# Kernel tuning notes

Measured on AMD Instinct MI355X. Metric: run time of the kernel, lower is better.

Reference implementation:

```python
import jax, jax.numpy as jnp
import numpy as np

SELF_OBS_DIM = 18
NBR_OBS_DIM = 6
NUM_NBR = 8
HID = 128

def _mlp2(x, W1, b1, W2, b2):
    return jnp.tanh(jnp.tanh(x @ W1 + b1) @ W2 + b2)

def setup_inputs() -> dict:
    key = jax.random.key(0)
    ks = jax.random.split(key, 20)
    B = 65536
    def w(k, i, o):
        return (jax.random.normal(k, (i, o), jnp.float32) / np.sqrt(i)).astype(jnp.float32)
    inp = {
        "self_obs": jax.random.normal(ks[0], (B, SELF_OBS_DIM), jnp.float32),
        "obs": jax.random.normal(ks[1], (B, SELF_OBS_DIM + NUM_NBR * NBR_OBS_DIM), jnp.float32),
        # embedding_mlp
        "e_W1": w(ks[2], SELF_OBS_DIM + NBR_OBS_DIM, HID), "e_b1": jnp.zeros((HID,), jnp.float32),
        "e_W2": w(ks[3], HID, HID), "e_b2": jnp.zeros((HID,), jnp.float32),
        # neighbor_value_mlp
        "v_W1": w(ks[4], HID, HID), "v_b1": jnp.zeros((HID,), jnp.float32),
        "v_W2": w(ks[5], HID, HID), "v_b2": jnp.zeros((HID,), jnp.float32),
        # attention_mlp
        "a_W1": w(ks[6], 2 * HID, HID), "a_b1": jnp.zeros((HID,), jnp.float32),
        "a_W2": w(ks[7], HID, HID), "a_b2": jnp.zeros((HID,), jnp.float32),
        "a_W3": w(ks[8], HID, 1), "a_b3": jnp.zeros((1,), jnp.float32),
        "all_neighbor_obs_size": NUM_NBR * NBR_OBS_DIM,
        "batch_size": B,
    }
    return inp

def reference(self_obs, obs, e_W1, e_b1, e_W2, e_b2, v_W1, v_b1, v_W2, v_b2,
              a_W1, a_b1, a_W2, a_b2, a_W3, a_b3, all_neighbor_obs_size, batch_size):
    B = batch_size
    n = NUM_NBR
    # slice out neighbor obs; reshape is batch-major: row index = b*n + k
    obs_nb = obs[:, SELF_OBS_DIM:SELF_OBS_DIM + all_neighbor_obs_size].reshape(-1, NBR_OBS_DIM)
    # torch .repeat(n, 1) tiles whole batch -> neighbor-major: row index = k*B + b (kept faithful)
    self_rep = jnp.tile(self_obs, (n, 1))
    emb = _mlp2(jnp.concatenate([self_rep, obs_nb], axis=1), e_W1, e_b1, e_W2, e_b2)  # [B*n, H]
    vals = _mlp2(emb, v_W1, v_b1, v_W2, v_b2)                                          # [B*n, H]
    emb_mean = emb.reshape(B, n, HID).mean(axis=1)                                     # [B, H]
    mean_rep = jnp.tile(emb_mean, (n, 1))                                              # [B*n, H]
    h = jnp.tanh(jnp.concatenate([emb, mean_rep], axis=1) @ a_W1 + a_b1)
    h = jnp.tanh(h @ a_W2 + a_b2)
    scores = (h @ a_W3 + a_b3).reshape(B, n)
    attn = jax.nn.softmax(scores, axis=1).reshape(-1, 1)
    out = (attn * vals).reshape(B, n, HID).sum(axis=1)                                 # [B, H]
    return out
```

## Files before the change

kernel.cpp:

```cpp
#include <hip/hip_runtime.h>
#include <math.h>

#define BATCH 65536
#define HID   128
#define NTHREADS 256

using bf16x8 = __attribute__((ext_vector_type(8))) short;
using f32x4  = __attribute__((ext_vector_type(4))) float;

#define E1H 0
#define E1L 4096
#define SWB 8192
#define BIASF 204800
#define MEANH 206592
#define WS_ELEMS_FULL (MEANH + BATCH*HID)

__device__ __forceinline__ float4 ld4(const float* p) { return *reinterpret_cast<const float4*>(p); }

__device__ __forceinline__ unsigned cvtpk(float a, float b) {
    unsigned r;
    asm("v_cvt_pk_bf16_f32 %0, %1, %2" : "=v"(r) : "v"(a), "v"(b));
    return r;
}

__device__ __forceinline__ float tanh_f(float x) {
    float t = __builtin_amdgcn_exp2f(x * 2.8853900817779268f);
    float r = __builtin_amdgcn_rcpf(t + 1.f);
    return 1.f - 2.f * r;
}

__device__ __forceinline__ f32x4 mfma16(bf16x8 a, bf16x8 b, f32x4 c) {
    return __builtin_amdgcn_mfma_f32_16x16x32_bf16(a, b, c, 0, 0, 0);
}

__device__ __forceinline__ bf16x8 pk8(unsigned u0, unsigned u1, unsigned u2, unsigned u3) {
    union { unsigned u[4]; bf16x8 v; } x;
    x.u[0] = u0; x.u[1] = u1; x.u[2] = u2; x.u[3] = u3;
    return x.v;
}

__device__ __forceinline__ void split_pack(float v0, float v1, float v2, float v3,
        unsigned& uh0, unsigned& uh1, unsigned& ul0, unsigned& ul1) {
    uh0 = cvtpk(v0, v1); uh1 = cvtpk(v2, v3);
    float f0 = __uint_as_float(uh0 << 16), f1 = __uint_as_float(uh0 & 0xffff0000u);
    float f2 = __uint_as_float(uh1 << 16), f3 = __uint_as_float(uh1 & 0xffff0000u);
    ul0 = cvtpk(v0 - f0, v1 - f1); ul1 = cvtpk(v2 - f2, v3 - f3);
}

__device__ __forceinline__ void zacc(f32x4 acc[2][8]) {
    #pragma unroll
    for (int rt = 0; rt < 2; ++rt)
        #pragma unroll
        for (int t = 0; t < 8; ++t) acc[rt][t] = f32x4{0.f, 0.f, 0.f, 0.f};
}

__device__ __forceinline__ int permc(int p) {
    return 32 * ((p >> 4) & 3) + 8 * ((p >> 2) & 3) + 4 * (p >> 6) + (p & 3);
}

__device__ __forceinline__ void gload16(const void* g, void* l) {
    __builtin_amdgcn_global_load_lds(
        (const __attribute__((address_space(1))) void*)g,
        (__attribute__((address_space(3))) void*)l, 16, 0, 0);
}
__device__ __forceinline__ void stage32k(short* dst, const short* __restrict__ src, int tid) {
    const char* g = (const char*)src + tid * 16;
    char* l = (char*)dst + tid * 16;
    #pragma unroll
    for (int s = 0; s < 8; ++s) gload16(g + s * 4096, l + s * 4096);
}

template<int NMUL>
__device__ __forceinline__ void mm_half(f32x4 acc[2][8],
        const bf16x8 Bh[2][4], const bf16x8 Bl[2][4],
        const short* W, int sE, int sO)
{
    #pragma unroll
    for (int tp = 0; tp < 4; ++tp) {
        const int t0 = 2 * tp, t1 = t0 + 1;
        __builtin_amdgcn_s_setprio(1);
        #pragma unroll
        for (int ks = 0; ks < 4; ++ks) {
            const int base = ((ks & 1) ? sO : sE) + (ks >> 1) * 64 + tp * 4096;
            bf16x8 w0 = *(const bf16x8*)(W + base);
            bf16x8 w1 = *(const bf16x8*)(W + base + 2048);
            acc[0][t0] = mfma16(w0, Bh[0][ks], acc[0][t0]);
            acc[0][t1] = mfma16(w1, Bh[0][ks], acc[0][t1]);
            acc[1][t0] = mfma16(w0, Bh[1][ks], acc[1][t0]);
            acc[1][t1] = mfma16(w1, Bh[1][ks], acc[1][t1]);
            if (NMUL == 2) {
                acc[0][t0] = mfma16(w0, Bl[0][ks], acc[0][t0]);
                acc[0][t1] = mfma16(w1, Bl[0][ks], acc[0][t1]);
                acc[1][t0] = mfma16(w0, Bl[1][ks], acc[1][t0]);
                acc[1][t1] = mfma16(w1, Bl[1][ks], acc[1][t1]);
            }
        }
        __builtin_amdgcn_s_setprio(0);
    }
}

__device__ __forceinline__ void mm_l1(f32x4 acc[2][8],
        const bf16x8 X0h[2], const bf16x8 X0l[2],
        const short* __restrict__ Wh, const short* __restrict__ Wl, int wb)
{
    #pragma unroll
    for (int tp = 0; tp < 4; ++tp) {
        const short* whp = Wh + wb + tp * 1024;
        const short* wlp = Wl + wb + tp * 1024;
        bf16x8 wh0 = *(const bf16x8*)(whp);
        bf16x8 wh1 = *(const bf16x8*)(whp + 512);
        bf16x8 wl0 = *(const bf16x8*)(wlp);
        bf16x8 wl1 = *(const bf16x8*)(wlp + 512);
        __builtin_amdgcn_s_setprio(1);
        acc[0][2*tp  ] = mfma16(wh0, X0h[0], acc[0][2*tp  ]);
        acc[0][2*tp+1] = mfma16(wh1, X0h[0], acc[0][2*tp+1]);
        acc[1][2*tp  ] = mfma16(wh0, X0h[1], acc[1][2*tp  ]);
        acc[1][2*tp+1] = mfma16(wh1, X0h[1], acc[1][2*tp+1]);
        acc[0][2*tp  ] = mfma16(wh0, X0l[0], acc[0][2*tp  ]);
        acc[0][2*tp+1] = mfma16(wh1, X0l[0], acc[0][2*tp+1]);
        acc[1][2*tp  ] = mfma16(wh0, X0l[1], acc[1][2*tp  ]);
        acc[1][2*tp+1] = mfma16(wh1, X0l[1], acc[1][2*tp+1]);
        acc[0][2*tp  ] = mfma16(wl0, X0h[0], acc[0][2*tp  ]);
        acc[0][2*tp+1] = mfma16(wl1, X0h[0], acc[0][2*tp+1]);
        acc[1][2*tp  ] = mfma16(wl0, X0h[1], acc[1][2*tp  ]);
        acc[1][2*tp+1] = mfma16(wl1, X0h[1], acc[1][2*tp+1]);
        __builtin_amdgcn_s_setprio(0);
    }
}

__device__ __forceinline__ void epi_state(const f32x4 acc[2][8], const float* __restrict__ bp,
        int q4, bf16x8 Nh[2][4], bf16x8 Nl[2][4])
{
    #pragma unroll
    for (int ks = 0; ks < 4; ++ks) {
        float4 b0 = ld4(bp + 16 * ks + q4);
        float4 b1 = ld4(bp + 16 * ks + 64 + q4);
        #pragma unroll
        for (int rt = 0; rt < 2; ++rt) {
            unsigned h0, h1, h2, h3, l0, l1, l2, l3;
            split_pack(tanh_f(acc[rt][ks][0] + b0.x), tanh_f(acc[rt][ks][1] + b0.y),
                       tanh_f(acc[rt][ks][2] + b0.z), tanh_f(acc[rt][ks][3] + b0.w),
                       h0, h1, l0, l1);
            split_pack(tanh_f(acc[rt][ks+4][0] + b1.x), tanh_f(acc[rt][ks+4][1] + b1.y),
                       tanh_f(acc[rt][ks+4][2] + b1.z), tanh_f(acc[rt][ks+4][3] + b1.w),
                       h2, h3, l2, l3);
            Nh[rt][ks] = pk8(h0, h1, h2, h3);
            Nl[rt][ks] = pk8(l0, l1, l2, l3);
        }
    }
}

__device__ __forceinline__ void epi_state_hi(const f32x4 acc[2][8], const float* __restrict__ bp,
        int q4, bf16x8 Nh[2][4])
{
    #pragma unroll
    for (int ks = 0; ks < 4; ++ks) {
        float4 b0 = ld4(bp + 16 * ks + q4);
        float4 b1 = ld4(bp + 16 * ks + 64 + q4);
        #pragma unroll
        for (int rt = 0; rt < 2; ++rt) {
            unsigned h0 = cvtpk(tanh_f(acc[rt][ks][0] + b0.x), tanh_f(acc[rt][ks][1] + b0.y));
            unsigned h1 = cvtpk(tanh_f(acc[rt][ks][2] + b0.z), tanh_f(acc[rt][ks][3] + b0.w));
            unsigned h2 = cvtpk(tanh_f(acc[rt][ks+4][0] + b1.x), tanh_f(acc[rt][ks+4][1] + b1.y));
            unsigned h3 = cvtpk(tanh_f(acc[rt][ks+4][2] + b1.z), tanh_f(acc[rt][ks+4][3] + b1.w));
            Nh[rt][ks] = pk8(h0, h1, h2, h3);
        }
    }
}

__device__ __forceinline__ void build_x0(bf16x8 X0h[2], bf16x8 X0l[2],
        const float* __restrict__ self_obs, const float* __restrict__ obs,
        int r0w, int lm, int q)
{
    #pragma unroll
    for (int rt = 0; rt < 2; ++rt) {
        int row = r0w + 16 * rt + lm;
        const float* sp = self_obs + (size_t)(row & (BATCH - 1)) * 18;
        float x0 = 0.f, x1 = 0.f, x2 = 0.f, x3 = 0.f, x4 = 0.f, x5 = 0.f, x6 = 0.f, x7 = 0.f;
        if (q == 0) {
            x0 = sp[0]; x1 = sp[1]; x2 = sp[2]; x3 = sp[3];
            x4 = sp[4]; x5 = sp[5]; x6 = sp[6]; x7 = sp[7];
        } else if (q == 1) {
            x0 = sp[8]; x1 = sp[9]; x2 = sp[10]; x3 = sp[11];
            x4 = sp[12]; x5 = sp[13]; x6 = sp[14]; x7 = sp[15];
        } else if (q == 2) {
            x0 = sp[16]; x1 = sp[17];
            const float* op = obs + (size_t)(row >> 3) * 66 + 18 + (row & 7) * 6;
            x2 = op[0]; x3 = op[1]; x4 = op[2]; x5 = op[3]; x6 = op[4]; x7 = op[5];
        }
        unsigned h0, h1, h2, h3, l0, l1, l2, l3;
        split_pack(x0, x1, x2, x3, h0, h1, l0, l1);
        split_pack(x4, x5, x6, x7, h2, h3, l2, l3);
        X0h[rt] = pk8(h0, h1, h2, h3);
        X0l[rt] = pk8(l0, l1, l2, l3);
    }
}

__device__ __forceinline__ int remap(int hw) {
    return (((hw >> 3) & 7) << 9) | ((hw & 7) << 6) | (hw >> 6);
}

__global__ void prep_w(const float* __restrict__ eW1, const float* __restrict__ eW2,
                       const float* __restrict__ vW1, const float* __restrict__ vW2,
                       const float* __restrict__ aW1, const float* __restrict__ aW2,
                       const float* __restrict__ eb1, const float* __restrict__ eb2,
                       const float* __restrict__ vb1, const float* __restrict__ vb2,
                       const float* __restrict__ ab1, const float* __restrict__ ab2,
                       const float* __restrict__ aW3,
                       short* __restrict__ ws)
{
    int t = blockIdx.x * blockDim.x + threadIdx.x;
    if (t >= 103296) return;
    if (t >= 102400) {
        int i = t - 102400, arr = i >> 7, p = i & 127;
        int c = permc(p);
        float v;
        if      (arr == 0) v = eb1[c];
        else if (arr == 1) v = eb2[c];
        else if (arr == 2) v = vb1[c];
        else if (arr == 3) v = vb2[c];
        else if (arr == 4) v = ab1[c];
        else if (arr == 5) v = ab2[c];
        else               v = aW3[c];
        ((float*)(ws + BIASF))[arr * 128 + p] = v;
        return;
    }
    float v; int dh, dl;
    if (t < 4096) {
        int p = t >> 5, k = t & 31;
        v = (k < 24) ? eW1[k * HID + permc(p)] : 0.f;
        dh = E1H + t; dl = E1L + t;
    } else {
        int u = t - 4096;
        int blob = u >> 14, vv = u & 16383;
        int p = vv >> 7;
        int k = (vv & 127) ^ ((p & 7) << 3);
        int c = permc(p);
        if      (blob == 0) v = eW2[k * HID + c];
        else if (blob == 1) v = aW1[k * HID + c];
        else if (blob == 2) v = aW1[(128 + k) * HID + c];
        else if (blob == 3) v = aW2[k * HID + c];
        else if (blob == 4) v = vW1[k * HID + c];
        else                v = vW2[k * HID + c];
        dh = SWB + blob * 32768 + vv;
        dl = dh + 16384;
    }
    unsigned uu = __float_as_uint(v);
    unsigned h = (uu + 0x7fffu + ((uu >> 16) & 1u)) >> 16;
    float lf = v - __uint_as_float(h << 16);
    ws[dh] = (short)h;
    ws[dl] = (short)(__float_as_uint(lf) >> 16);
}

__global__ __launch_bounds__(NTHREADS, 2)
void qk_mean(const float* __restrict__ self_obs, const float* __restrict__ obs,
             short* ws)
{
    __shared__ __align__(16) short B0[16384], B1[16384];
    const int tid = threadIdx.x, lane = tid & 63;
    const int lm = lane & 15, q = lane >> 4;
    const int r0w = remap(blockIdx.x) * 128 + (tid >> 6) * 32;
    const float* bf = (const float*)(ws + BIASF);
    const int sE = (lm * 128 + 8 * q) ^ ((lm & 7) << 3);
    const int sO = (lm * 128 + 8 * q + 32) ^ ((lm & 7) << 3);

    stage32k(B0, ws + SWB, tid);

    f32x4 acc[2][8];
    bf16x8 X0h[2], X0l[2];
    build_x0(X0h, X0l, self_obs, obs, r0w, lm, q);
    zacc(acc);
    mm_l1(acc, X0h, X0l, ws + E1H, ws + E1L, lm * 32 + q * 8);
    bf16x8 Hh[2][4], Hl[2][4];
    epi_state(acc, bf, q * 4, Hh, Hl);
    __syncthreads();

    stage32k(B1, ws + SWB + 16384, tid);
    zacc(acc);
    mm_half<2>(acc, Hh, Hl, B0, sE, sO);
    __syncthreads();
    mm_half<1>(acc, Hh, Hh, B1, sE, sO);

    const float* b2 = bf + 128;
    short* mh = ws + MEANH;
    #pragma unroll
    for (int rt = 0; rt < 2; ++rt) {
        float m[8][4];
        #pragma unroll
        for (int ks = 0; ks < 4; ++ks) {
            float4 b0 = ld4(b2 + 16 * ks + 4 * q);
            float4 b1 = ld4(b2 + 16 * ks + 64 + 4 * q);
            m[ks][0] = tanh_f(acc[rt][ks][0] + b0.x);
            m[ks][1] = tanh_f(acc[rt][ks][1] + b0.y);
            m[ks][2] = tanh_f(acc[rt][ks][2] + b0.z);
            m[ks][3] = tanh_f(acc[rt][ks][3] + b0.w);
            m[ks+4][0] = tanh_f(acc[rt][ks+4][0] + b1.x);
            m[ks+4][1] = tanh_f(acc[rt][ks+4][1] + b1.y);
            m[ks+4][2] = tanh_f(acc[rt][ks+4][2] + b1.z);
            m[ks+4][3] = tanh_f(acc[rt][ks+4][3] + b1.w);
        }
        #pragma unroll
        for (int t = 0; t < 8; ++t)
            #pragma unroll
            for (int e = 0; e < 4; ++e) {
                float v = m[t][e];
                v += __shfl_xor(v, 1); v += __shfl_xor(v, 2); v += __shfl_xor(v, 4);
                m[t][e] = v * 0.125f;
            }
        if ((lm & 7) == 0) {
            int g = (r0w >> 3) + 2 * rt + (lm >> 3);
            #pragma unroll
            for (int ks = 0; ks < 4; ++ks) {
                unsigned h0 = cvtpk(m[ks][0], m[ks][1]);
                unsigned h1 = cvtpk(m[ks][2], m[ks][3]);
                unsigned h2 = cvtpk(m[ks+4][0], m[ks+4][1]);
                unsigned h3 = cvtpk(m[ks+4][2], m[ks+4][3]);
                *(bf16x8*)(mh + (size_t)g * 128 + 32 * ks + 8 * q) = pk8(h0, h1, h2, h3);
            }
        }
    }
}

__global__ __launch_bounds__(NTHREADS, 2)
void qk_main(const float* __restrict__ self_obs, const float* __restrict__ obs,
             short* ws, float* __restrict__ out)
{
    __shared__ __align__(16) short B0[16384], B1[16384];
    const int tid = threadIdx.x, lane = tid & 63;
    const int lm = lane & 15, q = lane >> 4;
    const int r0w = remap(blockIdx.x) * 128 + (tid >> 6) * 32;
    const float* bf = (const float*)(ws + BIASF);
    const int sE = (lm * 128 + 8 * q) ^ ((lm & 7) << 3);
    const int sO = (lm * 128 + 8 * q + 32) ^ ((lm & 7) << 3);
    const short* W = ws + SWB;

    f32x4 acc[2][8];
    float a0, a1;

    stage32k(B0, W, tid);
    {
        bf16x8 X0h[2], X0l[2];
        build_x0(X0h, X0l, self_obs, obs, r0w, lm, q);
        zacc(acc);
        mm_l1(acc, X0h, X0l, ws + E1H, ws + E1L, lm * 32 + q * 8);
    }
    bf16x8 Hh[2][4], Hl[2][4];
    epi_state(acc, bf, q * 4, Hh, Hl);
    __syncthreads();

    stage32k(B1, W + 1 * 16384, tid);
    zacc(acc);
    mm_half<2>(acc, Hh, Hl, B0, sE, sO);
    __syncthreads();
    stage32k(B0, W + 2 * 16384, tid);
    mm_half<1>(acc, Hh, Hh, B1, sE, sO);
    bf16x8 Eh[2][4], El[2][4];
    epi_state(acc, bf + 128, q * 4, Eh, El);
    __syncthreads();

    stage32k(B1, W + 3 * 16384, tid);
    zacc(acc);
    mm_half<2>(acc, Eh, El, B0, sE, sO);
    __syncthreads();
    stage32k(B0, W + 4 * 16384, tid);
    bf16x8 Mh[2][4];
    {
        const short* mh = ws + MEANH;
        const size_t mr0 = (size_t)((r0w + lm) & (BATCH - 1)) * 128;
        const size_t mr1 = (size_t)((r0w + 16 + lm) & (BATCH - 1)) * 128;
        #pragma unroll
        for (int ks = 0; ks < 4; ++ks) {
            Mh[0][ks] = *(const bf16x8*)(mh + mr0 + 32 * ks + 8 * q);
            Mh[1][ks] = *(const bf16x8*)(mh + mr1 + 32 * ks + 8 * q);
        }
    }
    mm_half<1>(acc, Eh, Eh, B1, sE, sO);
    __syncthreads();

    stage32k(B1, W + 5 * 16384, tid);
    mm_half<1>(acc, Mh, Mh, B0, sE, sO);
    __syncthreads();
    stage32k(B0, W + 6 * 16384, tid);
    mm_half<1>(acc, Mh, Mh, B1, sE, sO);
    bf16x8 Ah[2][4];
    epi_state_hi(acc, bf + 4 * 128, q * 4, Ah);
    __syncthreads();

    stage32k(B1, W + 7 * 16384, tid);
    zacc(acc);
    mm_half<1>(acc, Ah, Ah, B0, sE, sO);
    __syncthreads();
    stage32k(B0, W + 8 * 16384, tid);
    mm_half<1>(acc, Ah, Ah, B1, sE, sO);
    {
        const float* b6  = bf + 5 * 128;
        const float* w3p = bf + 6 * 128;
        float p0 = 0.f, p1 = 0.f;
        #pragma unroll
        for (int t = 0; t < 8; ++t) {
            float4 b  = ld4(b6 + 16 * t + 4 * q);
            float4 wv = ld4(w3p + 16 * t + 4 * q);
            p0 += tanh_f(acc[0][t][0] + b.x) * wv.x + tanh_f(acc[0][t][1] + b.y) * wv.y
                + tanh_f(acc[0][t][2] + b.z) * wv.z + tanh_f(acc[0][t][3] + b.w) * wv.w;
            p1 += tanh_f(acc[1][t][0] + b.x) * wv.x + tanh_f(acc[1][t][1] + b.y) * wv.y
                + tanh_f(acc[1][t][2] + b.z) * wv.z + tanh_f(acc[1][t][3] + b.w) * wv.w;
        }
        p0 += __shfl_xor(p0, 16); p0 += __shfl_xor(p0, 32);
        p1 += __shfl_xor(p1, 16); p1 += __shfl_xor(p1, 32);
        float m0 = p0, m1 = p1;
        m0 = fmaxf(m0, __shfl_xor(m0, 1)); m0 = fmaxf(m0, __shfl_xor(m0, 2)); m0 = fmaxf(m0, __shfl_xor(m0, 4));
        m1 = fmaxf(m1, __shfl_xor(m1, 1)); m1 = fmaxf(m1, __shfl_xor(m1, 2)); m1 = fmaxf(m1, __shfl_xor(m1, 4));
        float e0 = __expf(p0 - m0), e1 = __expf(p1 - m1);
        float s0 = e0, s1 = e1;
        s0 += __shfl_xor(s0, 1); s0 += __shfl_xor(s0, 2); s0 += __shfl_xor(s0, 4);
        s1 += __shfl_xor(s1, 1); s1 += __shfl_xor(s1, 2); s1 += __shfl_xor(s1, 4);
        a0 = e0 * __builtin_amdgcn_rcpf(s0);
        a1 = e1 * __builtin_amdgcn_rcpf(s1);
    }
    __syncthreads();

    stage32k(B1, W + 9 * 16384, tid);
    zacc(acc);
    mm_half<2>(acc, Eh, El, B0, sE, sO);
    __syncthreads();
    stage32k(B0, W + 10 * 16384, tid);
    mm_half<1>(acc, Eh, Eh, B1, sE, sO);
    bf16x8 Vh[2][4], Vl[2][4];
    epi_state(acc, bf + 2 * 128, q * 4, Vh, Vl);
    __syncthreads();

    stage32k(B1, W + 11 * 16384, tid);
    zacc(acc);
    mm_half<2>(acc, Vh, Vl, B0, sE, sO);
    __syncthreads();
    mm_half<1>(acc, Vh, Vh, B1, sE, sO);
    const float* b4 = bf + 3 * 128;
    #pragma unroll
    for (int rt = 0; rt < 2; ++rt) {
        const float av = rt ? a1 : a0;
        float o[8][4];
        #pragma unroll
        for (int ks = 0; ks < 4; ++ks) {
            float4 b0 = ld4(b4 + 16 * ks + 4 * q);
            float4 b1 = ld4(b4 + 16 * ks + 64 + 4 * q);
            o[ks][0] = av * tanh_f(acc[rt][ks][0] + b0.x);
            o[ks][1] = av * tanh_f(acc[rt][ks][1] + b0.y);
            o[ks][2] = av * tanh_f(acc[rt][ks][2] + b0.z);
            o[ks][3] = av * tanh_f(acc[rt][ks][3] + b0.w);
            o[ks+4][0] = av * tanh_f(acc[rt][ks+4][0] + b1.x);
            o[ks+4][1] = av * tanh_f(acc[rt][ks+4][1] + b1.y);
            o[ks+4][2] = av * tanh_f(acc[rt][ks+4][2] + b1.z);
            o[ks+4][3] = av * tanh_f(acc[rt][ks+4][3] + b1.w);
        }
        #pragma unroll
        for (int t = 0; t < 8; ++t)
            #pragma unroll
            for (int e = 0; e < 4; ++e) {
                float v = o[t][e];
                v += __shfl_xor(v, 1); v += __shfl_xor(v, 2); v += __shfl_xor(v, 4);
                o[t][e] = v;
            }
        if ((lm & 7) == 0) {
            int g = (r0w >> 3) + 2 * rt + (lm >> 3);
            #pragma unroll
            for (int ks = 0; ks < 4; ++ks) {
                *(float4*)(out + (size_t)g * 128 + 32 * ks + 8 * q) =
                    make_float4(o[ks][0], o[ks][1], o[ks][2], o[ks][3]);
                *(float4*)(out + (size_t)g * 128 + 32 * ks + 8 * q + 4) =
                    make_float4(o[ks+4][0], o[ks+4][1], o[ks+4][2], o[ks+4][3]);
            }
        }
    }
}

extern "C" void kernel_launch(void* const* d_in, const int* in_sizes, int n_in,
                              void* d_out, int out_size, void* d_ws, size_t ws_size,
                              hipStream_t stream) {
    const float* self_obs = (const float*)d_in[0];
    const float* obs      = (const float*)d_in[1];
    const float* eW1 = (const float*)d_in[2];  const float* eb1 = (const float*)d_in[3];
    const float* eW2 = (const float*)d_in[4];  const float* eb2 = (const float*)d_in[5];
    const float* vW1 = (const float*)d_in[6];  const float* vb1 = (const float*)d_in[7];
    const float* vW2 = (const float*)d_in[8];  const float* vb2 = (const float*)d_in[9];
    const float* aW1 = (const float*)d_in[10]; const float* ab1 = (const float*)d_in[11];
    const float* aW2 = (const float*)d_in[12]; const float* ab2 = (const float*)d_in[13];
    const float* aW3 = (const float*)d_in[14];
    float* out = (float*)d_out;
    short* ws = (short*)d_ws;

    prep_w<<<404, 256, 0, stream>>>(eW1, eW2, vW1, vW2, aW1, aW2,
                                    eb1, eb2, vb1, vb2, ab1, ab2, aW3, ws);

    dim3 grid(4096);
    qk_mean<<<grid, NTHREADS, 0, stream>>>(self_obs, obs, ws);
    qk_main<<<grid, NTHREADS, 0, stream>>>(self_obs, obs, ws, out);
}
```

Measured before the change: 389.9 us.

## Split weight staging into quarter tiles to halve LDS in qk_mean

The qk_mean kernel now double-buffers weights in 16 KB quarter-layer chunks instead of 32 KB halves, so LDS per block drops from 64 KB to 32 KB. A new layer4/mm_q path overlaps each quarter's global-to-LDS load with the MFMA work on the previous quarter. This allows more resident blocks and finer overlap, at the cost of more barriers and more setprio toggling per layer.

```diff
diff --git a/kernel.cpp b/kernel.cpp
--- a/kernel.cpp
+++ b/kernel.cpp
@@ -63,11 +63,65 @@
         (const __attribute__((address_space(1))) void*)g,
         (__attribute__((address_space(3))) void*)l, 16, 0, 0);
 }
+__device__ __forceinline__ void stage16k(short* dst, const short* __restrict__ src, int tid) {
+    const char* g = (const char*)src + tid * 16;
+    char* l = (char*)dst + tid * 16;
+    #pragma unroll
+    for (int s = 0; s < 4; ++s) gload16(g + s * 4096, l + s * 4096);
+}
 __device__ __forceinline__ void stage32k(short* dst, const short* __restrict__ src, int tid) {
     const char* g = (const char*)src + tid * 16;
     char* l = (char*)dst + tid * 16;
     #pragma unroll
     for (int s = 0; s < 8; ++s) gload16(g + s * 4096, l + s * 4096);
+}
+
+template<int NMUL, int TPH>
+__device__ __forceinline__ void mm_q(f32x4 acc[2][8],
+        const bf16x8 Bh[2][4], const bf16x8 Bl[2][4],
+        const short* Wq, int sE, int sO)
+{
+    #pragma unroll
+    for (int tp = 0; tp < 2; ++tp) {
+        const int t0 = 4 * TPH + 2 * tp, t1 = t0 + 1;
+        #pragma unroll
+        for (int ks = 0; ks < 4; ++ks) {
+            const int base = ((ks & 1) ? sO : sE) + (ks >> 1) * 64 + tp * 4096;
+            bf16x8 w0 = *(const bf16x8*)(Wq + base);
+            bf16x8 w1 = *(const bf16x8*)(Wq + base + 2048);
+            __builtin_amdgcn_s_setprio(1);
+            acc[0][t0] = mfma16(w0, Bh[0][ks], acc[0][t0]);
+            acc[0][t1] = mfma16(w1, Bh[0][ks], acc[0][t1]);
+            acc[1][t0] = mfma16(w0, Bh[1][ks], acc[1][t0]);
+            acc[1][t1] = mfma16(w1, Bh[1][ks], acc[1][t1]);
+            if (NMUL == 2) {
+                acc[0][t0] = mfma16(w0, Bl[0][ks], acc[0][t0]);
+                acc[0][t1] = mfma16(w1, Bl[0][ks], acc[0][t1]);
+                acc[1][t0] = mfma16(w0, Bl[1][ks], acc[1][t0]);
+                acc[1][t1] = mfma16(w1, Bl[1][ks], acc[1][t1]);
+            }
+            __builtin_amdgcn_s_setprio(0);
+        }
+    }
+}
+
+template<int NH>
+__device__ __forceinline__ void layer4(f32x4 acc[2][8],
+        const bf16x8 Bh[2][4], const bf16x8 Bl[2][4],
+        short* B0, short* B1, const short* __restrict__ src,
+        const short* __restrict__ next, int sE, int sO, int tid)
+{
+    stage16k(B1, src + 8192, tid);
+    mm_q<NH, 0>(acc, Bh, Bl, B0, sE, sO);
+    __syncthreads();
+    stage16k(B0, src + 16384, tid);
+    mm_q<NH, 1>(acc, Bh, Bl, B1, sE, sO);
+    __syncthreads();
+    stage16k(B1, src + 24576, tid);
+    mm_q<1, 0>(acc, Bh, Bh, B0, sE, sO);
+    __syncthreads();
+    if (next) stage16k(B0, next, tid);
+    mm_q<1, 1>(acc, Bh, Bh, B1, sE, sO);
 }
 
 template<int NMUL>
@@ -256,7 +310,7 @@
 void qk_mean(const float* __restrict__ self_obs, const float* __restrict__ obs,
              short* ws)
 {
-    __shared__ __align__(16) short B0[16384], B1[16384];
+    __shared__ __align__(16) short B0[8192], B1[8192];
     const int tid = threadIdx.x, lane = tid & 63;
     const int lm = lane & 15, q = lane >> 4;
     const int r0w = remap(blockIdx.x) * 128 + (tid >> 6) * 32;
@@ -264,7 +318,7 @@
     const int sE = (lm * 128 + 8 * q) ^ ((lm & 7) << 3);
     const int sO = (lm * 128 + 8 * q + 32) ^ ((lm & 7) << 3);
 
-    stage32k(B0, ws + SWB, tid);
+    stage16k(B0, ws + SWB, tid);
 
     f32x4 acc[2][8];
     bf16x8 X0h[2], X0l[2];
@@ -275,11 +329,8 @@
     epi_state(acc, bf, q * 4, Hh, Hl);
     __syncthreads();
 
-    stage32k(B1, ws + SWB + 16384, tid);
-    zacc(acc);
-    mm_half<2>(acc, Hh, Hl, B0, sE, sO);
-    __syncthreads();
-    mm_half<1>(acc, Hh, Hh, B1, sE, sO);
+    zacc(acc);
+    layer4<2>(acc, Hh, Hl, B0, B1, ws + SWB, nullptr, sE, sO, tid);
 
     const float* b2 = bf + 128;
     short* mh = ws + MEANH;
```

Result: faster. 380.1 us (-2.5%).
